# Kernel tuning notes

Hardware: AMD Instinct MI355X
Metric: run time of the kernel (lower is better)

## Reference

```python
import jax, jax.numpy as jnp
import numpy as np

B, T, D, N = 4, 2048, 1024, 8
H = D // N


def _rope_tables(t, d, dtype=jnp.float32):
    inv_freq = 1.0 / (10000.0 ** (jnp.arange(0, d, 2, dtype=jnp.float32) / d))
    pos = jnp.arange(t, dtype=jnp.float32)
    ang = jnp.einsum('i,j->ij', pos, inv_freq)  # [T, D/2]
    cos = jnp.concatenate([jnp.cos(ang), jnp.cos(ang)], axis=-1).astype(dtype)  # [T, D]
    sin = jnp.concatenate([jnp.sin(ang), jnp.sin(ang)], axis=-1).astype(dtype)
    return cos, sin


def setup_inputs() -> dict:
    key = jax.random.key(0)
    kx, kq, kk, kv = jax.random.split(key, 4)
    s = 1.0 / np.sqrt(D)
    x = jax.random.normal(kx, (B, T, D), dtype=jnp.float32)
    wq = jax.random.normal(kq, (D, D), dtype=jnp.float32) * s
    wk = jax.random.normal(kk, (D, D), dtype=jnp.float32) * s
    wv = jax.random.normal(kv, (D, D), dtype=jnp.float32) * s
    cos, sin = _rope_tables(T, D)
    return {"x": x, "wq": wq, "wk": wk, "wv": wv, "cos": cos, "sin": sin}


def _rotate_half(z):
    # torch: view(..., -1, 2); x1=even idx, x2=odd idx; cat((-x2, x1), -1)
    return jnp.concatenate([-z[..., 1::2], z[..., 0::2]], axis=-1)


def reference(x, wq, wk, wv, cos, sin):
    b, t, c = x.shape
    n, h = N, H
    # nn.Linear(bias=False): y = x @ W.T
    q = jnp.einsum('btc,dc->btd', x, wq)
    k = jnp.einsum('btc,dc->btd', x, wk)
    v = jnp.einsum('btc,dc->btd', x, wv)
    q = q * cos + _rotate_half(q) * sin
    k = k * cos + _rotate_half(k) * sin
    q = q.reshape(b, t, n, h).transpose(0, 2, 1, 3)  # [b,n,t,h]
    k = k.reshape(b, t, n, h).transpose(0, 2, 1, 3)
    v = v.reshape(b, t, n, h).transpose(0, 2, 1, 3)
    scale = 1.0 / jnp.sqrt(jnp.asarray(h, dtype=q.dtype))
    scores = jnp.einsum('bnqh,bnkh->bnqk', q, k) * scale
    causal = jnp.tril(jnp.ones((t, t), dtype=bool))
    scores = jnp.where(causal, scores, jnp.finfo(scores.dtype).min)
    p = jax.nn.softmax(scores, axis=-1)
    out = jnp.einsum('bnqk,bnkh->bnqh', p, v)
    return out.transpose(0, 2, 1, 3).reshape(b, t, c)
```

## Files before the change

### kernel.cpp

```cpp
#include <hip/hip_runtime.h>

typedef unsigned short u16;
typedef unsigned int u32;
typedef _Float16 F16;
typedef __attribute__((ext_vector_type(8))) _Float16 h8v;
typedef __attribute__((ext_vector_type(4))) _Float16 h4v;
typedef __attribute__((ext_vector_type(4))) float f32x4;

#define DEV __device__ __forceinline__

DEV void gld16(const void* g, void* l) {
  __builtin_amdgcn_global_load_lds((const __attribute__((address_space(1))) void*)g,
                                   (__attribute__((address_space(3))) void*)l, 16, 0, 0);
}
DEV f32x4 mfma16(h8v a, h8v b, f32x4 c) {
  return __builtin_amdgcn_mfma_f32_16x16x32_f16(a, b, c, 0, 0, 0);
}

__global__ void __launch_bounds__(256) k_split_all(const float* __restrict__ x,
                                                   const float* __restrict__ wq,
                                                   const float* __restrict__ wk,
                                                   const float* __restrict__ wv,
                                                   F16* __restrict__ xh, F16* __restrict__ wh) {
  int i = blockIdx.x * 256 + threadIdx.x;
  const float* src; F16* dst; int li;
  if (i < 1048576)      { src = x;  dst = xh;            li = i; }
  else if (i < 1179648) { src = wq; dst = wh;            li = i - 1048576; }
  else if (i < 1310720) { src = wk; dst = wh + 1048576;  li = i - 1179648; }
  else                  { src = wv; dst = wh + 2097152;  li = i - 1310720; }
  const float4* p = (const float4*)src + (size_t)li * 2;
  float4 a = p[0], b = p[1];
  float v[8] = {a.x, a.y, a.z, a.w, b.x, b.y, b.z, b.w};
  h8v o;
#pragma unroll
  for (int j = 0; j < 8; ++j) o[j] = (F16)v[j];
  ((h8v*)dst)[li] = o;
}

__global__ void __launch_bounds__(256, 3) k_gemm_qkv(
    const F16* __restrict__ A, const F16* __restrict__ W,
    F16* __restrict__ qf, F16* __restrict__ kf, F16* __restrict__ vf) {
  __shared__ F16 lds[16384];
  F16* sA = lds;
  F16* sB = lds + 8192;
  const int tid = threadIdx.x;
  const int lane = tid & 63, w = tid >> 6;
  const int wm = w >> 1, wn = w & 1;
  const int l15 = lane & 15, g = lane >> 4;
  const int bid = blockIdx.x;
  const int mt = bid & 63, nt = bid >> 6;
  const F16* B = W + (size_t)(nt >> 3) * 1048576;
  F16* C = (nt < 8) ? qf : (nt < 16) ? kf : vf;
  const int m0 = mt * 128;
  const int n0 = (nt & 7) * 128;

  f32x4 acc[4][4] = {};

  for (int kt = 0; kt < 16; ++kt) {
    const int k0 = kt * 64;
#pragma unroll
    for (int p = 0; p < 4; ++p) {
      int u = p * 256 + tid;
      int row = u >> 3, jp = u & 7;
      int j = jp ^ (row & 7);
      size_t ga = (size_t)(m0 + row) * 1024 + k0 + j * 8;
      size_t gb = (size_t)(n0 + row) * 1024 + k0 + j * 8;
      gld16(A + ga, sA + u * 8);
      gld16(B + gb, sB + u * 8);
    }
    __syncthreads();
#pragma unroll
    for (int ks = 0; ks < 2; ++ks) {
      h8v fa[4], fb[4];
#pragma unroll
      for (int mf = 0; mf < 4; ++mf) {
        int row = wm * 64 + mf * 16 + l15;
        int off = row * 64 + (((ks * 4 + g) ^ (row & 7)) * 8);
        fa[mf] = *(const h8v*)(sA + off);
      }
#pragma unroll
      for (int nf = 0; nf < 4; ++nf) {
        int row = wn * 64 + nf * 16 + l15;
        int off = row * 64 + (((ks * 4 + g) ^ (row & 7)) * 8);
        fb[nf] = *(const h8v*)(sB + off);
      }
#pragma unroll
      for (int mf = 0; mf < 4; ++mf)
#pragma unroll
        for (int nf = 0; nf < 4; ++nf)
          acc[mf][nf] = mfma16(fa[mf], fb[nf], acc[mf][nf]);
    }
    __syncthreads();
  }
#pragma unroll
  for (int mf = 0; mf < 4; ++mf)
#pragma unroll
    for (int nf = 0; nf < 4; ++nf)
#pragma unroll
      for (int r = 0; r < 4; ++r) {
        int m = m0 + wm * 64 + mf * 16 + g * 4 + r;
        int n = n0 + wn * 64 + nf * 16 + l15;
        C[(size_t)m * 1024 + n] = (F16)acc[mf][nf][r];
      }
}

__global__ void __launch_bounds__(256) k_rope(const F16* __restrict__ zf,
                                              const float* __restrict__ cs, const float* __restrict__ sn,
                                              F16* __restrict__ zg, float scale) {
  const int bt = blockIdx.x;
  const int b = bt >> 11, t = bt & 2047;
  __shared__ float sz[1024];
  const int tid = threadIdx.x;
  {
    h4v zin = ((const h4v*)(zf + (size_t)bt * 1024))[tid];
#pragma unroll
    for (int j = 0; j < 4; ++j) sz[tid * 4 + j] = (float)zin[j];
  }
  __syncthreads();
  const int i0 = tid * 4;
  float4 c4 = ((const float4*)(cs + (size_t)t * 1024))[tid];
  float4 s4 = ((const float4*)(sn + (size_t)t * 1024))[tid];
  float cc[4] = {c4.x, c4.y, c4.z, c4.w};
  float ss[4] = {s4.x, s4.y, s4.z, s4.w};
  h4v ov;
#pragma unroll
  for (int j = 0; j < 4; ++j) {
    int i = i0 + j;
    float z;
    if (i < 512) z = sz[i] * cc[j] - sz[2 * i + 1] * ss[j];
    else         z = sz[i] * cc[j] + sz[2 * (i - 512)] * ss[j];
    ov[j] = (F16)(z * scale);
  }
  const int n = i0 >> 7, hh = i0 & 127;
  const size_t o = ((size_t)(b * 8 + n) * 2048 + t) * 128 + hh;
  *(h4v*)(zg + o) = ov;
}

__global__ void __launch_bounds__(256) k_vtrans(const F16* __restrict__ vf, F16* __restrict__ vt) {
  const int bid = blockIdx.x;
  const int tt = bid & 31, bn = bid >> 5;
  const int b = bn >> 3, n = bn & 7;
  const int t0 = tt * 64;
  __shared__ float s[64][129];
  const int tid = threadIdx.x;
#pragma unroll
  for (int r8 = 0; r8 < 4; ++r8) {
    int row = r8 * 16 + (tid >> 4);
    int c8 = tid & 15;
    h8v v = *(const h8v*)(vf + ((size_t)b * 2048 + t0 + row) * 1024 + n * 128 + c8 * 8);
#pragma unroll
    for (int k = 0; k < 8; ++k) s[row][c8 * 8 + k] = (float)v[k];
  }
  __syncthreads();
  const int h = tid >> 1, half = tid & 1;
  const size_t ob = ((size_t)bn * 128 + h) * 2048 + t0 + half * 32;
  h8v o[4];
#pragma unroll
  for (int j = 0; j < 32; ++j) o[j >> 3][j & 7] = (F16)s[half * 32 + j][h];
#pragma unroll
  for (int jj = 0; jj < 4; ++jj) *(h8v*)(vt + ob + jj * 8) = o[jj];
}

__global__ void __launch_bounds__(256, 4) k_attn(const F16* __restrict__ Q, const F16* __restrict__ K,
                                                 const F16* __restrict__ Vt, float* __restrict__ Out) {
  const int bid = blockIdx.x;
  const int bn = bid & 31;
  const int o = bid >> 5;
  int qt;
  if (o < 8)       qt = 31 - o;
  else if (o < 16) qt = o - 8;
  else if (o < 24) qt = 39 - o;
  else             qt = o - 16;
  const int b = bn >> 3, n = bn & 7;
  const int q0 = qt * 64;
  const int tid = threadIdx.x;
  const int lane = tid & 63, w = tid >> 6;
  const int l15 = lane & 15, g = lane >> 4;

  __shared__ F16 sm[16384];
  F16* sK = sm;
  F16* sV = sm + 8192;
  F16* sP = sK + w * 1024;

  h8v fq[4];
  {
    const size_t qoff = ((size_t)bn * 2048 + (q0 + w * 16 + l15)) * 128 + g * 8;
#pragma unroll
    for (int hs = 0; hs < 4; ++hs) fq[hs] = *(const h8v*)(Q + qoff + hs * 32);
  }

  f32x4 ot[8] = {};
  float mrun = -1e30f;
  float lrun = 0.f;

  const size_t kbase = (size_t)bn * 2048 * 128;
  const int nkv = qt + 1;

  for (int kv = 0; kv < nkv; ++kv) {
    const int k0 = kv * 64;
#pragma unroll
    for (int p = 0; p < 4; ++p) {
      int u = p * 256 + tid;
      { int row = u >> 4, jp = u & 15, j = jp ^ (row & 15);
        gld16(K + kbase + (size_t)(k0 + row) * 128 + j * 8, sK + u * 8); }
      { int row = u >> 3, jp = u & 7, j = jp ^ (row & 7);
        gld16(Vt + kbase + (size_t)row * 2048 + k0 + j * 8, sV + u * 8); }
    }
    __syncthreads();

    f32x4 st[4] = {};
#pragma unroll
    for (int f = 0; f < 4; ++f) {
      const int row = f * 16 + l15;
      const F16* bk = sK + row * 128;
#pragma unroll
      for (int hs = 0; hs < 4; ++hs) {
        const int j = (((hs * 4 + g) ^ (row & 15)) * 8);
        st[f] = mfma16(*(const h8v*)(bk + j), fq[hs], st[f]);
      }
    }
    __syncthreads();

    {
      const int qg = q0 + w * 16 + l15;
      if (k0 + 63 > q0 + w * 16) {
#pragma unroll
        for (int f = 0; f < 4; ++f)
#pragma unroll
          for (int r = 0; r < 4; ++r)
            if (k0 + f * 16 + g * 4 + r > qg) st[f][r] = -1e30f;
      }
      float tm = -1e30f;
#pragma unroll
      for (int f = 0; f < 4; ++f)
#pragma unroll
        for (int r = 0; r < 4; ++r) tm = fmaxf(tm, st[f][r]);
      tm = fmaxf(tm, __shfl_xor(tm, 16));
      tm = fmaxf(tm, __shfl_xor(tm, 32));
      const float mnew = fmaxf(mrun, tm);
      const float corr = exp2f(mrun - mnew);
      mrun = mnew;
      float ps = 0.f;
      const int q = l15;
#pragma unroll
      for (int f = 0; f < 4; ++f) {
        h4v p4;
#pragma unroll
        for (int r = 0; r < 4; ++r) {
          float p = exp2f(st[f][r] - mnew);
          ps += p;
          p4[r] = (F16)p;
        }
        const int off = q * 64 + (((2 * f + (g >> 1)) ^ (q & 7)) * 8) + (g & 1) * 4;
        *(h4v*)(sP + off) = p4;
      }
      ps += __shfl_xor(ps, 16);
      ps += __shfl_xor(ps, 32);
      lrun = lrun * corr + ps;
#pragma unroll
      for (int hf = 0; hf < 8; ++hf) {
        ot[hf][0] *= corr; ot[hf][1] *= corr;
        ot[hf][2] *= corr; ot[hf][3] *= corr;
      }
    }
    asm volatile("" ::: "memory");

    h8v fp[2];
    {
      const int q = l15;
#pragma unroll
      for (int c = 0; c < 2; ++c) {
        const int off = q * 64 + (((4 * c + g) ^ (q & 7)) * 8);
        fp[c] = *(const h8v*)(sP + off);
      }
    }
#pragma unroll
    for (int hf = 0; hf < 8; ++hf) {
      const int row = hf * 16 + l15;
      const int sw = row & 7;
#pragma unroll
      for (int c = 0; c < 2; ++c) {
        const int off = row * 64 + (((4 * c + g) ^ sw) * 8);
        ot[hf] = mfma16(*(const h8v*)(sV + off), fp[c], ot[hf]);
      }
    }
    __syncthreads();
  }

  {
    const float inv = 1.0f / lrun;
    const int qrow = q0 + w * 16 + l15;
    const size_t ob = ((size_t)b * 2048 + qrow) * 1024 + n * 128;
#pragma unroll
    for (int hf = 0; hf < 8; ++hf) {
      float4 o4;
      o4.x = ot[hf][0] * inv; o4.y = ot[hf][1] * inv;
      o4.z = ot[hf][2] * inv; o4.w = ot[hf][3] * inv;
      *(float4*)(Out + ob + hf * 16 + g * 4) = o4;
    }
  }
}

extern "C" void kernel_launch(void* const* d_in, const int* in_sizes, int n_in,
                              void* d_out, int out_size, void* d_ws, size_t ws_size,
                              hipStream_t stream) {
  const float* x  = (const float*)d_in[0];
  const float* wq = (const float*)d_in[1];
  const float* wk = (const float*)d_in[2];
  const float* wv = (const float*)d_in[3];
  const float* cs = (const float*)d_in[4];
  const float* sn = (const float*)d_in[5];
  float* out = (float*)d_out;

  F16* xh = (F16*)d_ws;
  F16* wh = xh + 8388608;
  F16* qf = wh + 3145728;
  F16* kf = qf + 8388608;
  F16* vf = kf + 8388608;
  F16* qg = xh;
  F16* kg = qf;
  F16* vtg = kf;

  if (ws_size < (size_t)73400320) return;

  const float QS = 0.08838834764831845f * 1.4426950408889634f;

  k_split_all<<<5632, 256, 0, stream>>>(x, wq, wk, wv, xh, wh);
  k_gemm_qkv<<<1536, 256, 0, stream>>>(xh, wh, qf, kf, vf);
  k_rope<<<8192, 256, 0, stream>>>(qf, cs, sn, qg, QS);
  k_rope<<<8192, 256, 0, stream>>>(kf, cs, sn, kg, 1.0f);
  k_vtrans<<<1024, 256, 0, stream>>>(vf, vtg);
  k_attn<<<1024, 256, 0, stream>>>(qg, kg, vtg, out);
}
```

Baseline: 265.0 us.

## Fuse RoPE and V transpose into one prep kernel; lazy softmax rescale in attention

Merges the two RoPE launches and the V-transpose launch into a single kernel that rotates Q and K together (sharing the cos/sin loads) and transposes V in extra blocks. K and V get their own workspace buffers so they no longer alias. In attention, P gets its own LDS region, which drops one barrier per KV tile; load addresses are precomputed and incremented; the online-softmax rescale is skipped unless the running max grows by more than 8 (log2 units). The lazy rescale lets probabilities reach up to 2^8 before normalisation, which adds fp16 range risk, and the larger LDS footprint may lower occupancy.

Result: faster. 257.6 us (-2.8%).

```diff
diff --git a/kernel.cpp b/kernel.cpp
--- a/kernel.cpp
+++ b/kernel.cpp
@@ -104,61 +104,69 @@
       }
 }
 
-__global__ void __launch_bounds__(256) k_rope(const F16* __restrict__ zf,
+__global__ void __launch_bounds__(256) k_prep(const F16* __restrict__ qf, const F16* __restrict__ kf,
+                                              const F16* __restrict__ vf,
                                               const float* __restrict__ cs, const float* __restrict__ sn,
-                                              F16* __restrict__ zg, float scale) {
-  const int bt = blockIdx.x;
-  const int b = bt >> 11, t = bt & 2047;
-  __shared__ float sz[1024];
+                                              F16* __restrict__ qg, F16* __restrict__ kg,
+                                              F16* __restrict__ vtg, float QS) {
+  __shared__ float smem[8256];
+  const int bid = blockIdx.x;
   const int tid = threadIdx.x;
-  {
-    h4v zin = ((const h4v*)(zf + (size_t)bt * 1024))[tid];
-#pragma unroll
-    for (int j = 0; j < 4; ++j) sz[tid * 4 + j] = (float)zin[j];
-  }
-  __syncthreads();
-  const int i0 = tid * 4;
-  float4 c4 = ((const float4*)(cs + (size_t)t * 1024))[tid];
-  float4 s4 = ((const float4*)(sn + (size_t)t * 1024))[tid];
-  float cc[4] = {c4.x, c4.y, c4.z, c4.w};
-  float ss[4] = {s4.x, s4.y, s4.z, s4.w};
-  h4v ov;
-#pragma unroll
-  for (int j = 0; j < 4; ++j) {
-    int i = i0 + j;
-    float z;
-    if (i < 512) z = sz[i] * cc[j] - sz[2 * i + 1] * ss[j];
-    else         z = sz[i] * cc[j] + sz[2 * (i - 512)] * ss[j];
-    ov[j] = (F16)(z * scale);
-  }
-  const int n = i0 >> 7, hh = i0 & 127;
-  const size_t o = ((size_t)(b * 8 + n) * 2048 + t) * 128 + hh;
-  *(h4v*)(zg + o) = ov;
-}
-
-__global__ void __launch_bounds__(256) k_vtrans(const F16* __restrict__ vf, F16* __restrict__ vt) {
-  const int bid = blockIdx.x;
-  const int tt = bid & 31, bn = bid >> 5;
-  const int b = bn >> 3, n = bn & 7;
-  const int t0 = tt * 64;
-  __shared__ float s[64][129];
-  const int tid = threadIdx.x;
-#pragma unroll
-  for (int r8 = 0; r8 < 4; ++r8) {
-    int row = r8 * 16 + (tid >> 4);
-    int c8 = tid & 15;
-    h8v v = *(const h8v*)(vf + ((size_t)b * 2048 + t0 + row) * 1024 + n * 128 + c8 * 8);
-#pragma unroll
-    for (int k = 0; k < 8; ++k) s[row][c8 * 8 + k] = (float)v[k];
-  }
-  __syncthreads();
-  const int h = tid >> 1, half = tid & 1;
-  const size_t ob = ((size_t)bn * 128 + h) * 2048 + t0 + half * 32;
-  h8v o[4];
-#pragma unroll
-  for (int j = 0; j < 32; ++j) o[j >> 3][j & 7] = (F16)s[half * 32 + j][h];
-#pragma unroll
-  for (int jj = 0; jj < 4; ++jj) *(h8v*)(vt + ob + jj * 8) = o[jj];
+  if (bid < 8192) {
+    float* sq = smem;
+    float* sk = smem + 1024;
+    const int b = bid >> 11, t = bid & 2047;
+    {
+      h4v qi = ((const h4v*)(qf + (size_t)bid * 1024))[tid];
+      h4v ki = ((const h4v*)(kf + (size_t)bid * 1024))[tid];
+#pragma unroll
+      for (int j = 0; j < 4; ++j) { sq[tid * 4 + j] = (float)qi[j]; sk[tid * 4 + j] = (float)ki[j]; }
+    }
+    __syncthreads();
+    const int i0 = tid * 4;
+    float4 c4 = ((const float4*)(cs + (size_t)t * 1024))[tid];
+    float4 s4 = ((const float4*)(sn + (size_t)t * 1024))[tid];
+    float cc[4] = {c4.x, c4.y, c4.z, c4.w};
+    float ss[4] = {s4.x, s4.y, s4.z, s4.w};
+    h4v qv, kv;
+#pragma unroll
+    for (int j = 0; j < 4; ++j) {
+      int i = i0 + j;
+      float zq, zk;
+      if (i < 512) { zq = sq[i] * cc[j] - sq[2 * i + 1] * ss[j];
+                     zk = sk[i] * cc[j] - sk[2 * i + 1] * ss[j]; }
+      else         { zq = sq[i] * cc[j] + sq[2 * (i - 512)] * ss[j];
+                     zk = sk[i] * cc[j] + sk[2 * (i - 512)] * ss[j]; }
+      qv[j] = (F16)(zq * QS);
+      kv[j] = (F16)zk;
+    }
+    const int n = i0 >> 7, hh = i0 & 127;
+    const size_t o = ((size_t)(b * 8 + n) * 2048 + t) * 128 + hh;
+    *(h4v*)(qg + o) = qv;
+    *(h4v*)(kg + o) = kv;
+  } else {
+    const int vb = bid - 8192;
+    const int tt = vb & 31, bn = vb >> 5;
+    const int b = bn >> 3, n = bn & 7;
+    const int t0 = tt * 64;
+    float (*s)[129] = (float(*)[129])smem;
+#pragma unroll
+    for (int r8 = 0; r8 < 4; ++r8) {
+      int row = r8 * 16 + (tid >> 4);
+      int c8 = tid & 15;
+      h8v v = *(const h8v*)(vf + ((size_t)b * 2048 + t0 + row) * 1024 + n * 128 + c8 * 8);
+#pragma unroll
+      for (int k = 0; k < 8; ++k) s[row][c8 * 8 + k] = (float)v[k];
+    }
+    __syncthreads();
+    const int h = tid >> 1, half = tid & 1;
+    const size_t ob = ((size_t)bn * 128 + h) * 2048 + t0 + half * 32;
+    h8v o[4];
+#pragma unroll
+    for (int j = 0; j < 32; ++j) o[j >> 3][j & 7] = (F16)s[half * 32 + j][h];
+#pragma unroll
+    for (int jj = 0; jj < 4; ++jj) *(h8v*)(vtg + ob + jj * 8) = o[jj];
+  }
 }
 
 __global__ void __launch_bounds__(256, 4) k_attn(const F16* __restrict__ Q, const F16* __restrict__ K,
@@ -177,10 +185,10 @@
   const int lane = tid & 63, w = tid >> 6;
   const int l15 = lane & 15, g = lane >> 4;
 
-  __shared__ F16 sm[16384];
+  __shared__ F16 sm[20480];
   F16* sK = sm;
   F16* sV = sm + 8192;
-  F16* sP = sK + w * 1024;
+  F16* sP = sm + 16384 + w * 1024;
 
   h8v fq[4];
   {
@@ -189,22 +197,32 @@
     for (int hs = 0; hs < 4; ++hs) fq[hs] = *(const h8v*)(Q + qoff + hs * 32);
   }
 
+  const size_t kbase = (size_t)bn * 2048 * 128;
+  const F16* kS[4]; const F16* vS[4]; F16* kD[4]; F16* vD[4];
+#pragma unroll
+  for (int p = 0; p < 4; ++p) {
+    int u = p * 256 + tid;
+    { int row = u >> 4, jp = u & 15, j = jp ^ (row & 15);
+      kS[p] = K + kbase + (size_t)row * 128 + j * 8;
+      kD[p] = sK + u * 8; }
+    { int row = u >> 3, jp = u & 7, j = jp ^ (row & 7);
+      vS[p] = Vt + kbase + (size_t)row * 2048 + j * 8;
+      vD[p] = sV + u * 8; }
+  }
+
   f32x4 ot[8] = {};
   float mrun = -1e30f;
   float lrun = 0.f;
-
-  const size_t kbase = (size_t)bn * 2048 * 128;
   const int nkv = qt + 1;
 
   for (int kv = 0; kv < nkv; ++kv) {
     const int k0 = kv * 64;
 #pragma unroll
     for (int p = 0; p < 4; ++p) {
-      int u = p * 256 + tid;
-      { int row = u >> 4, jp = u & 15, j = jp ^ (row & 15);
-        gld16(K + kbase + (size_t)(k0 + row) * 128 + j * 8, sK + u * 8); }
-      { int row = u >> 3, jp = u & 7, j = jp ^ (row & 7);
-        gld16(Vt + kbase + (size_t)row * 2048 + k0 + j * 8, sV + u * 8); }
+      gld16(kS[p], kD[p]);
+      gld16(vS[p], vD[p]);
+      kS[p] += 8192;
+      vS[p] += 64;
     }
     __syncthreads();
 
@@ -219,7 +237,6 @@
         st[f] = mfma16(*(const h8v*)(bk + j), fq[hs], st[f]);
       }
     }
-    __syncthreads();
 
     {
       const int qg = q0 + w * 16 + l15;
@@ -237,9 +254,13 @@
         for (int r = 0; r < 4; ++r) tm = fmaxf(tm, st[f][r]);
       tm = fmaxf(tm, __shfl_xor(tm, 16));
       tm = fmaxf(tm, __shfl_xor(tm, 32));
-      const float mnew = fmaxf(mrun, tm);
-      const float corr = exp2f(mrun - mnew);
-      mrun = mnew;
+      float corr = 1.f;
+      const bool resc = !__all(tm <= mrun + 8.0f);
+      if (resc) {
+        const float mn = fmaxf(mrun, tm);
+        corr = exp2f(mrun - mn);
+        mrun = mn;
+      }
       float ps = 0.f;
       const int q = l15;
 #pragma unroll
@@ -247,7 +268,7 @@
         h4v p4;
 #pragma unroll
         for (int r = 0; r < 4; ++r) {
-          float p = exp2f(st[f][r] - mnew);
+          float p = exp2f(st[f][r] - mrun);
           ps += p;
           p4[r] = (F16)p;
         }
@@ -257,10 +278,12 @@
       ps += __shfl_xor(ps, 16);
       ps += __shfl_xor(ps, 32);
       lrun = lrun * corr + ps;
-#pragma unroll
-      for (int hf = 0; hf < 8; ++hf) {
-        ot[hf][0] *= corr; ot[hf][1] *= corr;
-        ot[hf][2] *= corr; ot[hf][3] *= corr;
+      if (resc) {
+#pragma unroll
+        for (int hf = 0; hf < 8; ++hf) {
+          ot[hf][0] *= corr; ot[hf][1] *= corr;
+          ot[hf][2] *= corr; ot[hf][3] *= corr;
+        }
       }
     }
     asm volatile("" ::: "memory");
@@ -312,23 +335,21 @@
   const float* sn = (const float*)d_in[5];
   float* out = (float*)d_out;
 
-  F16* xh = (F16*)d_ws;
-  F16* wh = xh + 8388608;
-  F16* qf = wh + 3145728;
-  F16* kf = qf + 8388608;
-  F16* vf = kf + 8388608;
-  F16* qg = xh;
-  F16* kg = qf;
-  F16* vtg = kf;
-
-  if (ws_size < (size_t)73400320) return;
+  F16* xh  = (F16*)d_ws;
+  F16* wh  = xh + 8388608;
+  F16* qf  = wh + 3145728;
+  F16* kf  = qf + 8388608;
+  F16* vf  = kf + 8388608;
+  F16* kg  = vf + 8388608;
+  F16* vtg = kg + 8388608;
+  F16* qg  = xh;
+
+  if (ws_size < (size_t)106954752) return;
 
   const float QS = 0.08838834764831845f * 1.4426950408889634f;
 
   k_split_all<<<5632, 256, 0, stream>>>(x, wq, wk, wv, xh, wh);
   k_gemm_qkv<<<1536, 256, 0, stream>>>(xh, wh, qf, kf, vf);
-  k_rope<<<8192, 256, 0, stream>>>(qf, cs, sn, qg, QS);
-  k_rope<<<8192, 256, 0, stream>>>(kf, cs, sn, kg, 1.0f);
-  k_vtrans<<<1024, 256, 0, stream>>>(vf, vtg);
+  k_prep<<<9216, 256, 0, stream>>>(qf, kf, vf, cs, sn, qg, kg, vtg, QS);
   k_attn<<<1024, 256, 0, stream>>>(qg, kg, vtg, out);
 }
```
